# Optimization experiments

Measured on AMD Instinct MI355X. Metric: run time of the kernel, lower is better.

The kernel has to match this reference:

```python
import jax, jax.numpy as jnp
import numpy as np

# FIR kernel from resample_kernel=(1,3,3,1): outer product, normalized (gain=1)
_FIR_1D = np.array([1.0, 3.0, 3.0, 1.0], dtype=np.float32)
_FIR = np.outer(_FIR_1D, _FIR_1D)
_FIR = _FIR / _FIR.sum()  # 4x4


def setup_inputs() -> dict:
    key = jax.random.key(0)
    k1, k2, k3 = jax.random.split(key, 3)
    x = jax.random.normal(k1, (16, 256, 64, 64), dtype=jnp.float32)
    # fan_avg uniform init (default_init): variance = 1/fan_avg, fan_in=fan_out=256*9
    scale = float(np.sqrt(3.0 / (256 * 9)))
    w = jax.random.uniform(k2, (256, 256, 3, 3), dtype=jnp.float32, minval=-scale, maxval=scale)
    b = jax.random.normal(k3, (256,), dtype=jnp.float32) * 0.01
    return {"x": x, "w": w, "b": b}


def reference(x, w, b):
    # conv_downsample_2d: upfirdn2d(x, k, pad=(2,2)) then conv2d stride 2, then + bias
    B, C, H, W = x.shape
    # upfirdn2d with up=1, down=1 == zero-padded true convolution with k.
    # k is symmetric so flip is a no-op, but keep it for faithfulness.
    fir = jnp.asarray(_FIR[::-1, ::-1])                       # [4,4]
    fir_k = jnp.tile(fir[None, None, :, :], (C, 1, 1, 1))     # [C,1,4,4] depthwise
    x = jax.lax.conv_general_dilated(
        x, fir_k,
        window_strides=(1, 1),
        padding=((2, 2), (2, 2)),                             # (p+1)//2, p//2 with p=4
        feature_group_count=C,
        dimension_numbers=("NCHW", "OIHW", "NCHW"),
    )                                                          # [B,C,H+1,W+1]
    y = jax.lax.conv_general_dilated(
        x, w,
        window_strides=(2, 2),
        padding="VALID",
        dimension_numbers=("NCHW", "OIHW", "NCHW"),
    )                                                          # [B,outC,H//2,W//2]
    return y + b[None, :, None, None]
```

## Files before the change

### kernel.cpp

```cpp
#include <hip/hip_runtime.h>
#include <hip/hip_bf16.h>

typedef __attribute__((ext_vector_type(8))) short bf16x8;
typedef __attribute__((ext_vector_type(4))) float f32x4;
typedef __attribute__((ext_vector_type(8))) unsigned short u16x8;

#define KD 2304
#define PL 4232
#define OUT_PER_B (256 * 1024)

static __device__ __forceinline__ ushort f2bf(float f) {
  union { float f; unsigned int i; } v; v.f = f;
  unsigned int x = v.i;
  x += 0x7fffu + ((x >> 16) & 1u);
  return (ushort)(x >> 16);
}

#define GLDS16(gp, lp)                                                         \
  __builtin_amdgcn_global_load_lds(                                            \
      (const __attribute__((address_space(1))) void*)(gp),                     \
      (__attribute__((address_space(3))) void*)(lp), 16, 0, 0)

#define SWZ(g, r) (((g) & 8) | (((g) ^ (r)) & 7))

__global__ __launch_bounds__(256) void k_fir(const float* __restrict__ x,
                                             ushort* __restrict__ xfn,
                                             const float* __restrict__ w,
                                             ushort* __restrict__ wb) {
  __shared__ float sxp[64 * 76];
  __shared__ float stp[68 * 68];
  const int plane = blockIdx.x;
  const float* xp = x + (size_t)plane * 4096;
  ushort* op = xfn + (size_t)plane * PL;
  const int t = threadIdx.x;

  if (plane < 2304) {
    int iw = plane * 256 + t;
    float v = w[iw];
    int j = iw % 9;
    int t2 = iw / 9;
    int ic = t2 & 255;
    int oc = t2 >> 8;
    wb[oc * KD + j * 256 + ic] = f2bf(v);
  }

  {
    int r = t & 63, cs = t >> 6;
    int col = (cs < 2) ? (2 + cs) : (66 + cs);
    sxp[r * 76 + col] = 0.f;
  }
  for (int i = t; i < 272; i += 256) {
    int rr = i / 68, cc = i - rr * 68;
    int row = (rr < 2) ? rr : (64 + rr);
    stp[row * 68 + cc] = 0.f;
  }

  const float4* x4 = (const float4*)xp;
#pragma unroll
  for (int i = 0; i < 4; ++i) {
    int f4 = t + 256 * i;
    int r = f4 >> 4, w4 = f4 & 15;
    *(float4*)&sxp[r * 76 + 4 + w4 * 4] = x4[f4];
  }
  __syncthreads();

  for (int g = t; g < 1088; g += 256) {
    int i = g / 17, jg = g - i * 17;
    int j0 = jg << 2;
    const float* s = &sxp[i * 76 + j0];
    float4 a0 = *(const float4*)(s);
    float4 a1 = *(const float4*)(s + 4);
    float4 a2 = *(const float4*)(s + 8);
    float4 o;
    o.x = (a0.z + a1.y) + 3.f * (a0.w + a1.x);
    o.y = (a0.w + a1.z) + 3.f * (a1.x + a1.y);
    o.z = (a1.x + a1.w) + 3.f * (a1.y + a1.z);
    o.w = (a1.y + a2.x) + 3.f * (a1.z + a1.w);
    *(float4*)&stp[(i + 2) * 68 + j0] = o;
  }
  __syncthreads();

  for (int g = t; g < 1105; g += 256) {
    int i = g / 17, jg = g - i * 17;
    int j0 = jg << 2;
    const float* s = &stp[i * 68 + j0];
    float4 r0 = *(const float4*)(s);
    float4 r1 = *(const float4*)(s + 68);
    float4 r2 = *(const float4*)(s + 136);
    float4 r3 = *(const float4*)(s + 204);
    float4 o;
    o.x = (r0.x + r3.x) + 3.f * (r1.x + r2.x);
    o.y = (r0.y + r3.y) + 3.f * (r1.y + r2.y);
    o.z = (r0.z + r3.z) + 3.f * (r1.z + r2.z);
    o.w = (r0.w + r3.w) + 3.f * (r1.w + r2.w);
    ushort* q = op + i * 65 + j0;
    q[0] = f2bf(o.x * 0.015625f);
    if (j0 + 1 < 65) q[1] = f2bf(o.y * 0.015625f);
    if (j0 + 2 < 65) q[2] = f2bf(o.z * 0.015625f);
    if (j0 + 3 < 65) q[3] = f2bf(o.w * 0.015625f);
  }
}

__global__ __launch_bounds__(256) void k_tr(const ushort* __restrict__ xfn,
                                            ushort* __restrict__ xft) {
  __shared__ ushort ld[128 * 66];
  const int hw0 = blockIdx.x * 128;
  const int c0 = blockIdx.y * 64;
  const int b = blockIdx.z;
  const int t = threadIdx.x;

#pragma unroll
  for (int it = 0; it < 4; ++it) {
    int idx = it * 256 + t;
    int c = idx >> 4, q = idx & 15;
    u16x8 v = {};
    if (hw0 + q * 8 < 4225)
      v = *(const u16x8*)(xfn + (size_t)(b * 256 + c0 + c) * PL + hw0 + q * 8);
#pragma unroll
    for (int k = 0; k < 8; ++k)
      ld[(q * 8 + k) * 66 + (c ^ (k << 3))] = v[k];
  }
  __syncthreads();
#pragma unroll
  for (int it = 0; it < 4; ++it) {
    int idx = it * 256 + t;
    int hwl = idx >> 3, a = idx & 7;
    int k7 = hwl & 7;
    int hw = hw0 + hwl;
    if (hw < 4225) {
      u16x8 v = *(const u16x8*)&ld[hwl * 66 + ((a ^ k7) << 3)];
      *(u16x8*)&xft[((size_t)(b * 4225 + hw) << 8) + c0 + (a << 3)] = v;
    }
  }
}

__global__ __launch_bounds__(256) void k_gemm3(const ushort* __restrict__ Wb,
                                               const ushort* __restrict__ Xt,
                                               const float* __restrict__ bias,
                                               float* __restrict__ out) {
  __shared__ ushort lA[128 * 128];
  __shared__ ushort lB[64 * 128];
  const int bid = blockIdx.x;
  const int work = (bid & 7) * 64 + (bid >> 3);
  const int ntile = work >> 1;
  const int mtile = work & 1;
  const int m0 = mtile * 128;
  const int n0 = ntile * 64;
  const int t = threadIdx.x;
  const int wid = t >> 6, lane = t & 63;
  const int wm = wid >> 1, wn = wid & 1;
  const int lrow = lane & 15, kgrp = lane >> 4;

  const ushort* aB[8];
#pragma unroll
  for (int i = 0; i < 8; ++i) {
    int idx = i * 256 + t;
    int row = idx >> 4, gL = idx & 15;
    aB[i] = Wb + (size_t)(m0 + row) * KD + SWZ(gL, row) * 8;
  }
  const ushort* bB[4];
#pragma unroll
  for (int i = 0; i < 4; ++i) {
    int idx = i * 256 + t;
    int row = idx >> 4, gL = idx & 15;
    int n = n0 + row;
    int b = n >> 10, oh = (n >> 5) & 31, ow = n & 31;
    bB[i] = Xt + ((size_t)((b * 65 + 2 * oh) * 65 + 2 * ow) << 8) +
            SWZ(gL, row) * 8;
  }

  f32x4 acc[4][2];
#pragma unroll
  for (int i = 0; i < 4; ++i)
#pragma unroll
    for (int j = 0; j < 2; ++j) acc[i][j] = (f32x4){0.f, 0.f, 0.f, 0.f};

  for (int kt = 0; kt < 18; ++kt) {
    const int j = kt >> 1;
    const int dh = j / 3, dw = j - 3 * dh;
    const int boff = (dh * 65 + dw) * 256 + ((kt & 1) << 7);
    const int k0 = kt << 7;
    __syncthreads();
#pragma unroll
    for (int i = 0; i < 8; ++i)
      GLDS16(aB[i] + k0, &lA[(i * 256 + t) * 8]);
#pragma unroll
    for (int i = 0; i < 4; ++i)
      GLDS16(bB[i] + boff, &lB[(i * 256 + t) * 8]);
    __syncthreads();

#pragma unroll
    for (int s = 0; s < 4; ++s) {
      bf16x8 Af[4], Bf[2];
#pragma unroll
      for (int f = 0; f < 4; ++f) {
        int row = wm * 64 + f * 16 + lrow;
        Af[f] = *(const bf16x8*)&lA[row * 128 + SWZ(s * 4 + kgrp, row) * 8];
      }
#pragma unroll
      for (int f = 0; f < 2; ++f) {
        int row = wn * 32 + f * 16 + lrow;
        Bf[f] = *(const bf16x8*)&lB[row * 128 + SWZ(s * 4 + kgrp, row) * 8];
      }
#pragma unroll
      for (int fm = 0; fm < 4; ++fm)
#pragma unroll
        for (int fn = 0; fn < 2; ++fn)
          acc[fm][fn] = __builtin_amdgcn_mfma_f32_16x16x32_bf16(
              Af[fm], Bf[fn], acc[fm][fn], 0, 0, 0);
    }
  }

  f32x4 bv[4];
#pragma unroll
  for (int fm = 0; fm < 4; ++fm)
    bv[fm] = *(const f32x4*)(bias + m0 + wm * 64 + fm * 16 + kgrp * 4);

#pragma unroll
  for (int fm = 0; fm < 4; ++fm) {
#pragma unroll
    for (int fn = 0; fn < 2; ++fn) {
      int nn = n0 + wn * 32 + fn * 16 + lrow;
      int oc = m0 + wm * 64 + fm * 16 + kgrp * 4;
      float* op = out + (size_t)(nn >> 10) * OUT_PER_B + (nn & 1023) +
                  (size_t)oc * 1024;
      op[0]    = acc[fm][fn][0] + bv[fm][0];
      op[1024] = acc[fm][fn][1] + bv[fm][1];
      op[2048] = acc[fm][fn][2] + bv[fm][2];
      op[3072] = acc[fm][fn][3] + bv[fm][3];
    }
  }
}

extern "C" void kernel_launch(void* const* d_in, const int* in_sizes, int n_in,
                              void* d_out, int out_size, void* d_ws, size_t ws_size,
                              hipStream_t stream) {
  const float* x    = (const float*)d_in[0];
  const float* w    = (const float*)d_in[1];
  const float* bias = (const float*)d_in[2];
  float* out = (float*)d_out;

  char* ws = (char*)d_ws;
  ushort* xfn = (ushort*)ws;
  ushort* xft = (ushort*)(ws + 34668544);
  ushort* wb  = (ushort*)(ws + 34668544 + 34611200);

  k_fir<<<4096, 256, 0, stream>>>(x, xfn, w, wb);
  k_tr<<<dim3(34, 4, 16), 256, 0, stream>>>(xfn, xft);
  k_gemm3<<<512, 256, 0, stream>>>(wb, xft, bias, out);
}
```

Before: 69.50 us.

## Enlarge GEMM tile to 128x128 with intra-block split-K across two wave groups

The GEMM now uses 512-thread blocks computing 128x128 output tiles instead of 128x64, halving the grid to 256 blocks and reducing redundant weight loads. The two groups of four waves each handle half of every K stage, and their partial accumulators are summed through LDS before the bias add and store. Per-fragment LDS offsets are precomputed. This trades fewer blocks, which may underfill the 256 CUs, and an extra LDS reduction for better operand reuse per loaded byte.

Result: slower. 75.41 us (+8.5%).

```diff
diff --git a/kernel.cpp b/kernel.cpp
--- a/kernel.cpp
+++ b/kernel.cpp
@@ -134,100 +134,119 @@
   }
 }
 
-__global__ __launch_bounds__(256) void k_gemm3(const ushort* __restrict__ Wb,
+__global__ __launch_bounds__(512) void k_gemm3(const ushort* __restrict__ Wb,
                                                const ushort* __restrict__ Xt,
                                                const float* __restrict__ bias,
                                                float* __restrict__ out) {
-  __shared__ ushort lA[128 * 128];
-  __shared__ ushort lB[64 * 128];
+  __shared__ ushort lds[2 * 128 * 128];
+  ushort* lA = lds;
+  ushort* lB = lds + 128 * 128;
   const int bid = blockIdx.x;
-  const int work = (bid & 7) * 64 + (bid >> 3);
+  const int work = (bid & 7) * 32 + (bid >> 3);
   const int ntile = work >> 1;
   const int mtile = work & 1;
   const int m0 = mtile * 128;
-  const int n0 = ntile * 64;
+  const int n0 = ntile * 128;
   const int t = threadIdx.x;
   const int wid = t >> 6, lane = t & 63;
-  const int wm = wid >> 1, wn = wid & 1;
+  const int grp = wid >> 2;
+  const int wm = (wid >> 1) & 1, wn = wid & 1;
   const int lrow = lane & 15, kgrp = lane >> 4;
 
-  const ushort* aB[8];
-#pragma unroll
-  for (int i = 0; i < 8; ++i) {
-    int idx = i * 256 + t;
-    int row = idx >> 4, gL = idx & 15;
-    aB[i] = Wb + (size_t)(m0 + row) * KD + SWZ(gL, row) * 8;
-  }
+  const ushort* aB[4];
   const ushort* bB[4];
 #pragma unroll
   for (int i = 0; i < 4; ++i) {
-    int idx = i * 256 + t;
-    int row = idx >> 4, gL = idx & 15;
+    int idx = i * 512 + t;
+    int row = idx >> 4, g = idx & 15;
+    aB[i] = Wb + (size_t)(m0 + row) * KD + SWZ(g, row) * 8;
     int n = n0 + row;
     int b = n >> 10, oh = (n >> 5) & 31, ow = n & 31;
-    bB[i] = Xt + ((size_t)((b * 65 + 2 * oh) * 65 + 2 * ow) << 8) +
-            SWZ(gL, row) * 8;
-  }
-
-  f32x4 acc[4][2];
+    bB[i] = Xt + ((size_t)((b * 65 + 2 * oh) * 65 + 2 * ow) << 8) + SWZ(g, row) * 8;
+  }
+
+#define STAGE(st)                                                              \
+  {                                                                            \
+    const int j_ = (st) >> 1;                                                  \
+    const int dh_ = j_ / 3, dw_ = j_ - 3 * dh_;                                \
+    const int boff_ = (dh_ * 65 + dw_) * 256 + (((st) & 1) << 7);              \
+    const int k0_ = (st) << 7;                                                 \
+    _Pragma("unroll") for (int i_ = 0; i_ < 4; ++i_)                           \
+        GLDS16(aB[i_] + k0_, &lA[(i_ * 512 + t) * 8]);                         \
+    _Pragma("unroll") for (int i_ = 0; i_ < 4; ++i_)                           \
+        GLDS16(bB[i_] + boff_, &lB[(i_ * 512 + t) * 8]);                       \
+  }
+
+  int aOff[2][4], bOff[2][4];
+#pragma unroll
+  for (int f = 0; f < 4; ++f) {
+#pragma unroll
+    for (int s = 0; s < 2; ++s) {
+      int gA = grp * 8 + s * 4 + kgrp;
+      int arow = wm * 64 + f * 16 + lrow;
+      int brow = wn * 64 + f * 16 + lrow;
+      aOff[s][f] = arow * 128 + SWZ(gA, arow) * 8;
+      bOff[s][f] = brow * 128 + SWZ(gA, brow) * 8;
+    }
+  }
+
+  f32x4 acc[4][4];
 #pragma unroll
   for (int i = 0; i < 4; ++i)
 #pragma unroll
-    for (int j = 0; j < 2; ++j) acc[i][j] = (f32x4){0.f, 0.f, 0.f, 0.f};
-
-  for (int kt = 0; kt < 18; ++kt) {
-    const int j = kt >> 1;
-    const int dh = j / 3, dw = j - 3 * dh;
-    const int boff = (dh * 65 + dw) * 256 + ((kt & 1) << 7);
-    const int k0 = kt << 7;
+    for (int j = 0; j < 4; ++j) acc[i][j] = (f32x4){0.f, 0.f, 0.f, 0.f};
+
+  for (int st = 0; st < 18; ++st) {
     __syncthreads();
-#pragma unroll
-    for (int i = 0; i < 8; ++i)
-      GLDS16(aB[i] + k0, &lA[(i * 256 + t) * 8]);
-#pragma unroll
-    for (int i = 0; i < 4; ++i)
-      GLDS16(bB[i] + boff, &lB[(i * 256 + t) * 8]);
+    STAGE(st);
     __syncthreads();
-
-#pragma unroll
-    for (int s = 0; s < 4; ++s) {
-      bf16x8 Af[4], Bf[2];
+#pragma unroll
+    for (int s = 0; s < 2; ++s) {
+      bf16x8 Af[4], Bf[4];
 #pragma unroll
       for (int f = 0; f < 4; ++f) {
-        int row = wm * 64 + f * 16 + lrow;
-        Af[f] = *(const bf16x8*)&lA[row * 128 + SWZ(s * 4 + kgrp, row) * 8];
+        Af[f] = *(const bf16x8*)&lA[aOff[s][f]];
+        Bf[f] = *(const bf16x8*)&lB[bOff[s][f]];
       }
 #pragma unroll
-      for (int f = 0; f < 2; ++f) {
-        int row = wn * 32 + f * 16 + lrow;
-        Bf[f] = *(const bf16x8*)&lB[row * 128 + SWZ(s * 4 + kgrp, row) * 8];
-      }
-#pragma unroll
       for (int fm = 0; fm < 4; ++fm)
 #pragma unroll
-        for (int fn = 0; fn < 2; ++fn)
+        for (int fn = 0; fn < 4; ++fn)
           acc[fm][fn] = __builtin_amdgcn_mfma_f32_16x16x32_bf16(
               Af[fm], Bf[fn], acc[fm][fn], 0, 0, 0);
     }
   }
 
-  f32x4 bv[4];
-#pragma unroll
-  for (int fm = 0; fm < 4; ++fm)
-    bv[fm] = *(const f32x4*)(bias + m0 + wm * 64 + fm * 16 + kgrp * 4);
-
-#pragma unroll
-  for (int fm = 0; fm < 4; ++fm) {
-#pragma unroll
-    for (int fn = 0; fn < 2; ++fn) {
-      int nn = n0 + wn * 32 + fn * 16 + lrow;
-      int oc = m0 + wm * 64 + fm * 16 + kgrp * 4;
-      float* op = out + (size_t)(nn >> 10) * OUT_PER_B + (nn & 1023) +
-                  (size_t)oc * 1024;
-      op[0]    = acc[fm][fn][0] + bv[fm][0];
-      op[1024] = acc[fm][fn][1] + bv[fm][1];
-      op[2048] = acc[fm][fn][2] + bv[fm][2];
-      op[3072] = acc[fm][fn][3] + bv[fm][3];
+  __syncthreads();
+  float* rbase = (float*)lds + (wm * 2 + wn) * 4096;
+  if (grp == 1) {
+#pragma unroll
+    for (int fm = 0; fm < 4; ++fm)
+#pragma unroll
+      for (int fn = 0; fn < 4; ++fn)
+        *(f32x4*)&rbase[(fm * 4 + fn) * 256 + lane * 4] = acc[fm][fn];
+  }
+  __syncthreads();
+  if (grp == 0) {
+    f32x4 bv[4];
+#pragma unroll
+    for (int fm = 0; fm < 4; ++fm)
+      bv[fm] = *(const f32x4*)(bias + m0 + wm * 64 + fm * 16 + kgrp * 4);
+#pragma unroll
+    for (int fm = 0; fm < 4; ++fm) {
+#pragma unroll
+      for (int fn = 0; fn < 4; ++fn) {
+        f32x4 other = *(const f32x4*)&rbase[(fm * 4 + fn) * 256 + lane * 4];
+        f32x4 r = acc[fm][fn] + other;
+        int nn = n0 + wn * 64 + fn * 16 + lrow;
+        int oc = m0 + wm * 64 + fm * 16 + kgrp * 4;
+        float* op = out + (size_t)(nn >> 10) * OUT_PER_B + (nn & 1023) +
+                    (size_t)oc * 1024;
+        op[0]    = r[0] + bv[fm][0];
+        op[1024] = r[1] + bv[fm][1];
+        op[2048] = r[2] + bv[fm][2];
+        op[3072] = r[3] + bv[fm][3];
+      }
     }
   }
 }
@@ -247,5 +266,5 @@
 
   k_fir<<<4096, 256, 0, stream>>>(x, xfn, w, wb);
   k_tr<<<dim3(34, 4, 16), 256, 0, stream>>>(xfn, xft);
-  k_gemm3<<<512, 256, 0, stream>>>(wb, xft, bias, out);
-}
+  k_gemm3<<<256, 512, 0, stream>>>(wb, xft, bias, out);
+}
```

## Fuse FIR blur and channel-last transpose into one banded ring-buffer kernel

Applied to the files above, without the earlier changes.

Replaces the separate FIR kernel and transpose kernel with one kernel. Each block handles a 13-row output band for 64 channels, streams input rows through LDS and keeps a 4-row ring of horizontally filtered bf16 rows. It applies the vertical filter from that ring and writes channel-last bf16 data directly for the GEMM. This removes the write and re-read of the intermediate planar buffer, but launches only 320 blocks with a serial 17-step loop and two barriers per step. The horizontal result is now rounded to bf16 before the vertical pass.

Result: slower. 71.84 us (+3.4%).

```diff
diff --git a/kernel.cpp b/kernel.cpp
--- a/kernel.cpp
+++ b/kernel.cpp
@@ -6,7 +6,6 @@
 typedef __attribute__((ext_vector_type(8))) unsigned short u16x8;
 
 #define KD 2304
-#define PL 4232
 #define OUT_PER_B (256 * 1024)
 
 static __device__ __forceinline__ ushort f2bf(float f) {
@@ -15,6 +14,9 @@
   x += 0x7fffu + ((x >> 16) & 1u);
   return (ushort)(x >> 16);
 }
+static __device__ __forceinline__ float bf2f(ushort u) {
+  union { unsigned int i; float f; } v; v.i = ((unsigned)u) << 16; return v.f;
+}
 
 #define GLDS16(gp, lp)                                                         \
   __builtin_amdgcn_global_load_lds(                                            \
@@ -23,114 +25,108 @@
 
 #define SWZ(g, r) (((g) & 8) | (((g) ^ (r)) & 7))
 
-__global__ __launch_bounds__(256) void k_fir(const float* __restrict__ x,
-                                             ushort* __restrict__ xfn,
-                                             const float* __restrict__ w,
-                                             ushort* __restrict__ wb) {
-  __shared__ float sxp[64 * 76];
-  __shared__ float stp[68 * 68];
-  const int plane = blockIdx.x;
-  const float* xp = x + (size_t)plane * 4096;
-  ushort* op = xfn + (size_t)plane * PL;
-  const int t = threadIdx.x;
-
-  if (plane < 2304) {
-    int iw = plane * 256 + t;
-    float v = w[iw];
-    int j = iw % 9;
-    int t2 = iw / 9;
-    int ic = t2 & 255;
-    int oc = t2 >> 8;
-    wb[oc * KD + j * 256 + ic] = f2bf(v);
-  }
-
-  {
-    int r = t & 63, cs = t >> 6;
-    int col = (cs < 2) ? (2 + cs) : (66 + cs);
-    sxp[r * 76 + col] = 0.f;
-  }
-  for (int i = t; i < 272; i += 256) {
-    int rr = i / 68, cc = i - rr * 68;
-    int row = (rr < 2) ? rr : (64 + rr);
-    stp[row * 68 + cc] = 0.f;
-  }
-
-  const float4* x4 = (const float4*)xp;
-#pragma unroll
-  for (int i = 0; i < 4; ++i) {
-    int f4 = t + 256 * i;
-    int r = f4 >> 4, w4 = f4 & 15;
-    *(float4*)&sxp[r * 76 + 4 + w4 * 4] = x4[f4];
-  }
-  __syncthreads();
-
-  for (int g = t; g < 1088; g += 256) {
-    int i = g / 17, jg = g - i * 17;
-    int j0 = jg << 2;
-    const float* s = &sxp[i * 76 + j0];
-    float4 a0 = *(const float4*)(s);
-    float4 a1 = *(const float4*)(s + 4);
-    float4 a2 = *(const float4*)(s + 8);
-    float4 o;
-    o.x = (a0.z + a1.y) + 3.f * (a0.w + a1.x);
-    o.y = (a0.w + a1.z) + 3.f * (a1.x + a1.y);
-    o.z = (a1.x + a1.w) + 3.f * (a1.y + a1.z);
-    o.w = (a1.y + a2.x) + 3.f * (a1.z + a1.w);
-    *(float4*)&stp[(i + 2) * 68 + j0] = o;
-  }
-  __syncthreads();
-
-  for (int g = t; g < 1105; g += 256) {
-    int i = g / 17, jg = g - i * 17;
-    int j0 = jg << 2;
-    const float* s = &stp[i * 68 + j0];
-    float4 r0 = *(const float4*)(s);
-    float4 r1 = *(const float4*)(s + 68);
-    float4 r2 = *(const float4*)(s + 136);
-    float4 r3 = *(const float4*)(s + 204);
-    float4 o;
-    o.x = (r0.x + r3.x) + 3.f * (r1.x + r2.x);
-    o.y = (r0.y + r3.y) + 3.f * (r1.y + r2.y);
-    o.z = (r0.z + r3.z) + 3.f * (r1.z + r2.z);
-    o.w = (r0.w + r3.w) + 3.f * (r1.w + r2.w);
-    ushort* q = op + i * 65 + j0;
-    q[0] = f2bf(o.x * 0.015625f);
-    if (j0 + 1 < 65) q[1] = f2bf(o.y * 0.015625f);
-    if (j0 + 2 < 65) q[2] = f2bf(o.z * 0.015625f);
-    if (j0 + 3 < 65) q[3] = f2bf(o.w * 0.015625f);
-  }
-}
-
-__global__ __launch_bounds__(256) void k_tr(const ushort* __restrict__ xfn,
-                                            ushort* __restrict__ xft) {
-  __shared__ ushort ld[128 * 66];
-  const int hw0 = blockIdx.x * 128;
+__global__ __launch_bounds__(256) void k_fir2(const float* __restrict__ x,
+                                              ushort* __restrict__ xft,
+                                              const float* __restrict__ wsrc,
+                                              ushort* __restrict__ wb) {
+  __shared__ float sx[64 * 76];
+  __shared__ ushort ring[4 * 65 * 72];
+  const int band = blockIdx.x;
   const int c0 = blockIdx.y * 64;
   const int b = blockIdx.z;
+  const int r0 = band * 13;
   const int t = threadIdx.x;
 
-#pragma unroll
-  for (int it = 0; it < 4; ++it) {
-    int idx = it * 256 + t;
-    int c = idx >> 4, q = idx & 15;
-    u16x8 v = {};
-    if (hw0 + q * 8 < 4225)
-      v = *(const u16x8*)(xfn + (size_t)(b * 256 + c0 + c) * PL + hw0 + q * 8);
-#pragma unroll
-    for (int k = 0; k < 8; ++k)
-      ld[(q * 8 + k) * 66 + (c ^ (k << 3))] = v[k];
-  }
-  __syncthreads();
-#pragma unroll
-  for (int it = 0; it < 4; ++it) {
-    int idx = it * 256 + t;
-    int hwl = idx >> 3, a = idx & 7;
-    int k7 = hwl & 7;
-    int hw = hw0 + hwl;
-    if (hw < 4225) {
-      u16x8 v = *(const u16x8*)&ld[hwl * 66 + ((a ^ k7) << 3)];
-      *(u16x8*)&xft[((size_t)(b * 4225 + hw) << 8) + c0 + (a << 3)] = v;
-    }
+  {
+    int flat = band + 5 * (blockIdx.y + 4 * b);
+    for (int iw = flat * 256 + t; iw < 589824; iw += 81920) {
+      float v = wsrc[iw];
+      int j = iw % 9;
+      int t2 = iw / 9;
+      int ic = t2 & 255, oc = t2 >> 8;
+      wb[oc * KD + j * 256 + ic] = f2bf(v);
+    }
+  }
+
+  {
+    int r = t >> 2, cs = t & 3;
+    sx[r * 76 + (cs < 2 ? 2 + cs : 66 + cs)] = 0.f;
+  }
+
+  for (int it = 0; it < 17; ++it) {
+    const int ir = r0 - 2 + it;
+
+    float4 rg[4];
+    if (it <= 15) {
+      if (ir >= 0 && ir < 64) {
+#pragma unroll
+        for (int i = 0; i < 4; ++i) {
+          int f4 = i * 256 + t;
+          int c = f4 >> 4, q = f4 & 15;
+          rg[i] = *(const float4*)(x +
+                    ((size_t)((b * 256 + c0 + c) * 64 + ir) << 6) + q * 4);
+        }
+      } else {
+#pragma unroll
+        for (int i = 0; i < 4; ++i) rg[i] = make_float4(0.f, 0.f, 0.f, 0.f);
+      }
+    }
+
+    if (it >= 4) {
+      const int o = r0 - 4 + it;
+#pragma unroll
+      for (int i2 = 0; i2 < 3; ++i2) {
+        int idx = i2 * 256 + t;
+        if (idx < 520) {
+          int w = idx >> 3, a = idx & 7;
+          u16x8 r4[4];
+#pragma unroll
+          for (int d = 0; d < 4; ++d) {
+            int slot = (o - 2 + d) & 3;
+            r4[d] = *(const u16x8*)&ring[(slot * 65 + w) * 72 + a * 8];
+          }
+          u16x8 ov;
+#pragma unroll
+          for (int k = 0; k < 8; ++k) {
+            float f0 = bf2f(r4[0][k]), f1 = bf2f(r4[1][k]);
+            float f2 = bf2f(r4[2][k]), f3 = bf2f(r4[3][k]);
+            ov[k] = f2bf(((f0 + f3) + 3.f * (f1 + f2)) * 0.015625f);
+          }
+          *(u16x8*)&xft[((size_t)(b * 4225 + o * 65 + w) << 8) + c0 + a * 8] = ov;
+        }
+      }
+    }
+
+    if (it <= 15) {
+#pragma unroll
+      for (int i = 0; i < 4; ++i) {
+        int f4 = i * 256 + t;
+        int c = f4 >> 4, q = f4 & 15;
+        *(float4*)&sx[c * 76 + 4 + q * 4] = rg[i];
+      }
+    }
+    __syncthreads();
+
+    if (it <= 15) {
+      ushort* rw = ring + (ir & 3) * 65 * 72;
+#pragma unroll
+      for (int i2 = 0; i2 < 5; ++i2) {
+        int idx = i2 * 256 + t;
+        if (idx < 1088) {
+          int g = idx >> 6, c = idx & 63;
+          const float* s = &sx[c * 76 + g * 4];
+          float4 a0 = *(const float4*)(s);
+          float4 a1 = *(const float4*)(s + 4);
+          float4 a2 = *(const float4*)(s + 8);
+          int w0 = g * 4;
+          rw[w0 * 72 + c] = f2bf((a0.z + a1.y) + 3.f * (a0.w + a1.x));
+          if (w0 + 1 < 65) rw[(w0 + 1) * 72 + c] = f2bf((a0.w + a1.z) + 3.f * (a1.x + a1.y));
+          if (w0 + 2 < 65) rw[(w0 + 2) * 72 + c] = f2bf((a1.x + a1.w) + 3.f * (a1.y + a1.z));
+          if (w0 + 3 < 65) rw[(w0 + 3) * 72 + c] = f2bf((a1.y + a2.x) + 3.f * (a1.z + a1.w));
+        }
+      }
+    }
+    __syncthreads();
   }
 }
 
@@ -241,11 +237,9 @@
   float* out = (float*)d_out;
 
   char* ws = (char*)d_ws;
-  ushort* xfn = (ushort*)ws;
-  ushort* xft = (ushort*)(ws + 34668544);
-  ushort* wb  = (ushort*)(ws + 34668544 + 34611200);
-
-  k_fir<<<4096, 256, 0, stream>>>(x, xfn, w, wb);
-  k_tr<<<dim3(34, 4, 16), 256, 0, stream>>>(xfn, xft);
+  ushort* xft = (ushort*)ws;
+  ushort* wb  = (ushort*)(ws + 34611200);
+
+  k_fir2<<<dim3(5, 4, 16), 256, 0, stream>>>(x, xft, w, wb);
   k_gemm3<<<512, 256, 0, stream>>>(wb, xft, bias, out);
 }
```
